# Optimization experiments

Hardware: AMD Instinct MI355X
Metric: run time of the kernel (lower is better)

## Reference

```python
import jax, jax.numpy as jnp
import numpy as np

SPEED_OF_SOUND = 343.0
SAMPLING_FREQUENCY = 96000.0
CROP_LENGTH = 256


def setup_inputs() -> dict:
    key = jax.random.key(0)
    k1, k2, k3, k4 = jax.random.split(key, 4)
    B1, B2, R, T = 4, 1024, 64, 16384
    recordings = jax.random.normal(k1, (B1, R, T), dtype=jnp.float32)
    sample_locations = jax.random.uniform(k2, (B1, B2, 3), dtype=jnp.float32)  # points in unit cube
    emitter_location = jnp.array([0.0, 0.0, 0.5], dtype=jnp.float32)
    receiver_locations = jax.random.uniform(k3, (R, 3), dtype=jnp.float32) * 0.2
    canonical_echo = jax.random.normal(k4, (CROP_LENGTH,), dtype=jnp.float32)
    return {
        "recordings": recordings,
        "sample_locations": sample_locations,
        "emitter_location": emitter_location,
        "receiver_locations": receiver_locations,
        "canonical_echo": canonical_echo,
    }


def _time_of_flight_crop(recordings, sample_locations, emitter_location, receiver_locations):
    # recordings: (B1, R, T); sample_locations: (B1, B2, 3)
    B1, R, T = recordings.shape
    # emitter -> sample distance: (B1, B2)
    d_es = jnp.linalg.norm(sample_locations - emitter_location, axis=-1)
    # sample -> receiver distance: (B1, B2, R)
    d_sr = jnp.linalg.norm(
        sample_locations[:, :, None, :] - receiver_locations[None, None, :, :], axis=-1
    )
    # fractional start sample index of the echo window: (B1, B2, R)
    start = (d_es[:, :, None] + d_sr) / SPEED_OF_SOUND * SAMPLING_FREQUENCY
    # fractional sample indices for the crop window: (B1, B2, R, L)
    idx = start[..., None] + jnp.arange(CROP_LENGTH, dtype=recordings.dtype)
    i0f = jnp.floor(idx)
    frac = idx - i0f
    i0 = jnp.clip(i0f.astype(jnp.int32), 0, T - 1)
    i1 = jnp.clip(i0 + 1, 0, T - 1)
    # gather per (B1, R) row: vmap over B2 so we never broadcast recordings to (B1,B2,R,T)
    gather = jax.vmap(
        lambda i: jnp.take_along_axis(recordings, i, axis=-1), in_axes=1, out_axes=1
    )
    v0 = gather(i0)  # (B1, B2, R, L)
    v1 = gather(i1)
    return v0 * (1.0 - frac) + v1 * frac  # linear interpolation


def reference(recordings, sample_locations, emitter_location, receiver_locations, canonical_echo):
    cropped = _time_of_flight_crop(
        recordings, sample_locations, emitter_location, receiver_locations
    )  # (B1, B2, R, L)
    # dot with canonical echo template over L, clamp at 0, sum over receivers
    products = jnp.einsum("bqrl,l->bqr", cropped, canonical_echo)
    products = jnp.maximum(products, 0.0)
    magnitude = jnp.sum(products, axis=2)  # (B1, B2)
    return magnitude
```

## Files before the change

kernel.cpp:

```cpp
#include <hip/hip_runtime.h>

#define T_LEN 16384
#define R_CNT 64
#define CROP 256
#define B2_CNT 1024
#define QS 128
#define CDW 584
#define CDW_S 656

typedef _Float16 h2 __attribute__((ext_vector_type(2)));

__device__ __forceinline__ h2 as_h2(unsigned u) {
    union { unsigned u; h2 h; } v; v.u = u; return v.h;
}

#if __has_builtin(__builtin_amdgcn_fdot2)
__device__ __forceinline__ float DOT2(unsigned a, unsigned b, float c) {
    return __builtin_amdgcn_fdot2(as_h2(a), as_h2(b), c, false);
}
#else
__device__ __forceinline__ float DOT2(unsigned a, unsigned b, float c) {
    h2 x = as_h2(a), y = as_h2(b);
    return fmaf((float)x[0], (float)y[0], fmaf((float)x[1], (float)y[1], c));
}
#endif

__global__ void zero_out(float* __restrict__ out) {
    out[blockIdx.x * 256 + threadIdx.x] = 0.0f;
}

__global__ __launch_bounds__(256, 6) void tof_kernel(
    const float* __restrict__ recordings,
    const float* __restrict__ sample_locations,
    const float* __restrict__ emitter,
    const float* __restrict__ receivers,
    const float* __restrict__ echo,
    float* __restrict__ out)
{
    const int blk  = blockIdx.x;
    const int b1   = blk >> 9;
    const int r    = (blk >> 3) & 63;
    const int qc   = blk & 7;
    const int tid  = threadIdx.x;
    const int lane = tid & 63;
    const int wave = tid >> 6;
    const int i8   = lane & 7;
    const int g3   = lane >> 3;

    __shared__ unsigned s_copy[8 * CDW_S];
    __shared__ unsigned s_echo_pk[CROP / 2];
    __shared__ float2   s_sf[QS];

    const float* __restrict__ row = recordings + ((size_t)b1 * R_CNT + r) * T_LEN;
    #pragma unroll
    for (int c = 0; c < 8; ++c)
        for (int j = tid; j < CDW; j += 256) {
            const float a = row[c + 2 * j];
            const float b = row[c + 2 * j + 1];
            s_copy[c * CDW_S + j + 4 * (j >> 5)] =
                __builtin_bit_cast(unsigned, __builtin_amdgcn_cvt_pkrtz(a, b));
        }

    if (tid < CROP / 2)
        s_echo_pk[tid] = __builtin_bit_cast(unsigned,
            __builtin_amdgcn_cvt_pkrtz(echo[2 * tid], echo[2 * tid + 1]));

    if (tid < QS) {
        const int q = qc * QS + tid;
        const float sx = sample_locations[(b1 * B2_CNT + q) * 3 + 0];
        const float sy = sample_locations[(b1 * B2_CNT + q) * 3 + 1];
        const float sz = sample_locations[(b1 * B2_CNT + q) * 3 + 2];
        const float ex = emitter[0], ey = emitter[1], ez = emitter[2];
        const float dex = sx - ex, dey = sy - ey, dez = sz - ez;
        const float d_es = sqrtf(fmaf(dex, dex, fmaf(dey, dey, dez * dez)));
        const float rx = receivers[r * 3 + 0];
        const float ry = receivers[r * 3 + 1];
        const float rz = receivers[r * 3 + 2];
        const float dx = sx - rx, dy = sy - ry, dz = sz - rz;
        const float d_sr = sqrtf(fmaf(dx, dx, fmaf(dy, dy, dz * dz)));

        const float SCALE = 96000.0f / 343.0f;
        const float start = (d_es + d_sr) * SCALE;
        const float i0f   = floorf(start);
        int s0 = (int)i0f;
        s0 = s0 < 0 ? 0 : (s0 > 904 ? 904 : s0);
        s_sf[tid] = make_float2(__int_as_float(s0), start - i0f);
    }
    __syncthreads();

    unsigned e[16];
    #pragma unroll
    for (int n = 0; n < 4; ++n)
        *(uint4*)&e[4 * n] = *(const uint4*)&s_echo_pk[i8 * 16 + 4 * n];

    for (int pass = 0; pass < 4; ++pass) {
        const int ql = wave * 32 + pass * 8 + g3;
        const float2 sf  = s_sf[ql];
        const int   s0   = __float_as_int(sf.x);
        const float frac = sf.y;
        const int   c    = s0 & 7;
        const int   D    = 4 * (s0 >> 3) + 16 * i8;

        const unsigned* __restrict__ cb = &s_copy[c * CDW_S];

        unsigned d[17];
        #pragma unroll
        for (int n = 0; n < 4; ++n) {
            const int dj = D + 4 * n;
            *(uint4*)&d[4 * n] = *(const uint4*)&cb[dj + 4 * (dj >> 5)];
        }
        {
            const int dj = D + 16;
            d[16] = cb[dj + 4 * (dj >> 5)];
        }

        float A = 0.0f, B = 0.0f;
        #pragma unroll
        for (int k = 0; k < 16; ++k) {
            A = DOT2(e[k], d[k], A);
            const unsigned sh = (d[k] >> 16) | (d[k + 1] << 16);
            B = DOT2(e[k], sh, B);
        }

        float pr = fmaf(frac, B - A, A);
        pr += __shfl_xor(pr, 1);
        pr += __shfl_xor(pr, 2);
        pr += __shfl_xor(pr, 4);

        if (i8 == 0)
            atomicAdd(&out[b1 * B2_CNT + qc * QS + ql], fmaxf(pr, 0.0f));
    }
}

extern "C" void kernel_launch(void* const* d_in, const int* in_sizes, int n_in,
                              void* d_out, int out_size, void* d_ws, size_t ws_size,
                              hipStream_t stream) {
    const float* recordings       = (const float*)d_in[0];
    const float* sample_locations = (const float*)d_in[1];
    const float* emitter          = (const float*)d_in[2];
    const float* receivers        = (const float*)d_in[3];
    const float* echo             = (const float*)d_in[4];
    float* out                    = (float*)d_out;

    const int B1 = in_sizes[1] / (B2_CNT * 3);

    zero_out<<<dim3(B1 * B2_CNT / 256), dim3(256), 0, stream>>>(out);
    tof_kernel<<<dim3(B1 * R_CNT * 8), dim3(256), 0, stream>>>(
        recordings, sample_locations, emitter, receivers, echo, out);
}
```

Measured before the change: 84.54 us.

## Precompute per-row echo correlation at all lags, then interpolate per sample pair

Interpolation is linear, so the dot product of the echo with an interpolated crop equals the interpolation of two integer-lag correlations. A first kernel computes the correlation of each (b1, r) recording row with the echo at every lag 0..919 and writes it to workspace. A second kernel computes each sample's time of flight and reads two correlation values per receiver. The second kernel sums receivers in shared memory instead of with atomics, which also removes the zero-out launch. The work now scales with the number of lags rather than the number of samples, at the cost of a global round trip through the workspace and a second kernel launch.

```diff
diff --git a/kernel.cpp b/kernel.cpp
--- a/kernel.cpp
+++ b/kernel.cpp
@@ -4,9 +4,9 @@
 #define R_CNT 64
 #define CROP 256
 #define B2_CNT 1024
-#define QS 128
-#define CDW 584
-#define CDW_S 656
+#define CDW 588
+#define CDW_S 664
+#define NLAG 928
 
 typedef _Float16 h2 __attribute__((ext_vector_type(2)));
 
@@ -25,31 +25,23 @@
 }
 #endif
 
-__global__ void zero_out(float* __restrict__ out) {
-    out[blockIdx.x * 256 + threadIdx.x] = 0.0f;
-}
-
-__global__ __launch_bounds__(256, 6) void tof_kernel(
+__global__ __launch_bounds__(256) void corr_kernel(
     const float* __restrict__ recordings,
-    const float* __restrict__ sample_locations,
-    const float* __restrict__ emitter,
-    const float* __restrict__ receivers,
     const float* __restrict__ echo,
-    float* __restrict__ out)
+    float* __restrict__ C)
 {
     const int blk  = blockIdx.x;
-    const int b1   = blk >> 9;
-    const int r    = (blk >> 3) & 63;
-    const int qc   = blk & 7;
+    const int b1   = blk >> 8;
+    const int r    = (blk >> 2) & 63;
+    const int base = (blk & 3) * 256;
     const int tid  = threadIdx.x;
     const int lane = tid & 63;
     const int wave = tid >> 6;
     const int i8   = lane & 7;
     const int g3   = lane >> 3;
 
-    __shared__ unsigned s_copy[8 * CDW_S];
-    __shared__ unsigned s_echo_pk[CROP / 2];
-    __shared__ float2   s_sf[QS];
+    __shared__ __align__(16) unsigned s_copy[8 * CDW_S];
+    __shared__ __align__(16) unsigned s_echo_pk[CROP / 2];
 
     const float* __restrict__ row = recordings + ((size_t)b1 * R_CNT + r) * T_LEN;
     #pragma unroll
@@ -60,32 +52,9 @@
             s_copy[c * CDW_S + j + 4 * (j >> 5)] =
                 __builtin_bit_cast(unsigned, __builtin_amdgcn_cvt_pkrtz(a, b));
         }
-
     if (tid < CROP / 2)
         s_echo_pk[tid] = __builtin_bit_cast(unsigned,
             __builtin_amdgcn_cvt_pkrtz(echo[2 * tid], echo[2 * tid + 1]));
-
-    if (tid < QS) {
-        const int q = qc * QS + tid;
-        const float sx = sample_locations[(b1 * B2_CNT + q) * 3 + 0];
-        const float sy = sample_locations[(b1 * B2_CNT + q) * 3 + 1];
-        const float sz = sample_locations[(b1 * B2_CNT + q) * 3 + 2];
-        const float ex = emitter[0], ey = emitter[1], ez = emitter[2];
-        const float dex = sx - ex, dey = sy - ey, dez = sz - ez;
-        const float d_es = sqrtf(fmaf(dex, dex, fmaf(dey, dey, dez * dez)));
-        const float rx = receivers[r * 3 + 0];
-        const float ry = receivers[r * 3 + 1];
-        const float rz = receivers[r * 3 + 2];
-        const float dx = sx - rx, dy = sy - ry, dz = sz - rz;
-        const float d_sr = sqrtf(fmaf(dx, dx, fmaf(dy, dy, dz * dz)));
-
-        const float SCALE = 96000.0f / 343.0f;
-        const float start = (d_es + d_sr) * SCALE;
-        const float i0f   = floorf(start);
-        int s0 = (int)i0f;
-        s0 = s0 < 0 ? 0 : (s0 > 904 ? 904 : s0);
-        s_sf[tid] = make_float2(__int_as_float(s0), start - i0f);
-    }
     __syncthreads();
 
     unsigned e[16];
@@ -93,42 +62,101 @@
     for (int n = 0; n < 4; ++n)
         *(uint4*)&e[4 * n] = *(const uint4*)&s_echo_pk[i8 * 16 + 4 * n];
 
+    const int s = wave * 8 + g3;
+    float* __restrict__ Crow = C + ((size_t)b1 * R_CNT + r) * NLAG;
+
+    #pragma unroll
     for (int pass = 0; pass < 4; ++pass) {
-        const int ql = wave * 32 + pass * 8 + g3;
-        const float2 sf  = s_sf[ql];
-        const int   s0   = __float_as_int(sf.x);
-        const float frac = sf.y;
-        const int   c    = s0 & 7;
-        const int   D    = 4 * (s0 >> 3) + 16 * i8;
+        const int J = base + pass * 64 + (s & 7) + ((s >> 3) * 16);
+        if (J < 920) {
+            const int c = J & 7;
+            const int b = J >> 3;
+            const unsigned* __restrict__ cb = &s_copy[c * CDW_S];
 
-        const unsigned* __restrict__ cb = &s_copy[c * CDW_S];
+            unsigned d[20];
+            #pragma unroll
+            for (int n = 0; n < 5; ++n) {
+                const int dj = 4 * b + 16 * i8 + 4 * n;
+                *(uint4*)&d[4 * n] = *(const uint4*)&cb[dj + 4 * (dj >> 5)];
+            }
 
-        unsigned d[17];
+            float a0 = 0.0f, a1 = 0.0f;
+            #pragma unroll
+            for (int k = 0; k < 16; ++k) {
+                a0 = DOT2(e[k], d[k],     a0);
+                a1 = DOT2(e[k], d[k + 4], a1);
+            }
+            a0 += __shfl_xor(a0, 1); a1 += __shfl_xor(a1, 1);
+            a0 += __shfl_xor(a0, 2); a1 += __shfl_xor(a1, 2);
+            a0 += __shfl_xor(a0, 4); a1 += __shfl_xor(a1, 4);
+            if (i8 == 0) {
+                Crow[J]     = a0;
+                Crow[J + 8] = a1;
+            }
+        }
+    }
+}
+
+__global__ __launch_bounds__(256) void pair_kernel(
+    const float* __restrict__ sample_locations,
+    const float* __restrict__ emitter,
+    const float* __restrict__ receivers,
+    const float* __restrict__ C,
+    float* __restrict__ out)
+{
+    const int blk = blockIdx.x;
+    const int b1  = blk >> 6;
+    const int qc  = blk & 63;
+    const int tid = threadIdx.x;
+    const int ql  = tid & 15;
+    const int rg  = tid >> 4;
+
+    __shared__ float s_recv[R_CNT * 3];
+    __shared__ float s_part[16][17];
+
+    if (tid < R_CNT * 3) s_recv[tid] = receivers[tid];
+    __syncthreads();
+
+    const int q = qc * 16 + ql;
+    const float sx = sample_locations[(b1 * B2_CNT + q) * 3 + 0];
+    const float sy = sample_locations[(b1 * B2_CNT + q) * 3 + 1];
+    const float sz = sample_locations[(b1 * B2_CNT + q) * 3 + 2];
+    const float ex = emitter[0], ey = emitter[1], ez = emitter[2];
+    const float dex = sx - ex, dey = sy - ey, dez = sz - ez;
+    const float d_es = sqrtf(fmaf(dex, dex, fmaf(dey, dey, dez * dez)));
+
+    const float SCALE = 96000.0f / 343.0f;
+    float acc = 0.0f;
+
+    #pragma unroll
+    for (int rr = 0; rr < 4; ++rr) {
+        const int r = rg * 4 + rr;
+        const float rx = s_recv[r * 3 + 0];
+        const float ry = s_recv[r * 3 + 1];
+        const float rz = s_recv[r * 3 + 2];
+        const float dx = sx - rx, dy = sy - ry, dz = sz - rz;
+        const float d_sr = sqrtf(fmaf(dx, dx, fmaf(dy, dy, dz * dz)));
+
+        const float start = (d_es + d_sr) * SCALE;
+        const float i0f   = floorf(start);
+        const float frac  = start - i0f;
+        int s0 = (int)i0f;
+        s0 = s0 < 0 ? 0 : (s0 > 904 ? 904 : s0);
+
+        const float* cp = C + ((size_t)b1 * R_CNT + r) * NLAG + s0;
+        const float c0 = cp[0];
+        const float c1 = cp[1];
+        acc += fmaxf(fmaf(frac, c1 - c0, c0), 0.0f);
+    }
+
+    s_part[rg][ql] = acc;
+    __syncthreads();
+
+    if (tid < 16) {
+        float sum = 0.0f;
         #pragma unroll
-        for (int n = 0; n < 4; ++n) {
-            const int dj = D + 4 * n;
-            *(uint4*)&d[4 * n] = *(const uint4*)&cb[dj + 4 * (dj >> 5)];
-        }
-        {
-            const int dj = D + 16;
-            d[16] = cb[dj + 4 * (dj >> 5)];
-        }
-
-        float A = 0.0f, B = 0.0f;
-        #pragma unroll
-        for (int k = 0; k < 16; ++k) {
-            A = DOT2(e[k], d[k], A);
-            const unsigned sh = (d[k] >> 16) | (d[k + 1] << 16);
-            B = DOT2(e[k], sh, B);
-        }
-
-        float pr = fmaf(frac, B - A, A);
-        pr += __shfl_xor(pr, 1);
-        pr += __shfl_xor(pr, 2);
-        pr += __shfl_xor(pr, 4);
-
-        if (i8 == 0)
-            atomicAdd(&out[b1 * B2_CNT + qc * QS + ql], fmaxf(pr, 0.0f));
+        for (int g = 0; g < 16; ++g) sum += s_part[g][tid];
+        out[b1 * B2_CNT + qc * 16 + tid] = sum;
     }
 }
 
@@ -141,10 +169,11 @@
     const float* receivers        = (const float*)d_in[3];
     const float* echo             = (const float*)d_in[4];
     float* out                    = (float*)d_out;
+    float* C                      = (float*)d_ws;
 
     const int B1 = in_sizes[1] / (B2_CNT * 3);
 
-    zero_out<<<dim3(B1 * B2_CNT / 256), dim3(256), 0, stream>>>(out);
-    tof_kernel<<<dim3(B1 * R_CNT * 8), dim3(256), 0, stream>>>(
-        recordings, sample_locations, emitter, receivers, echo, out);
+    corr_kernel<<<dim3(B1 * R_CNT * 4), dim3(256), 0, stream>>>(recordings, echo, C);
+    pair_kernel<<<dim3(B1 * 64), dim3(256), 0, stream>>>(sample_locations, emitter,
+                                                         receivers, C, out);
 }
```

After: 77.70 us. 8.1% less time.

## Precompute per-row cross-correlation lags and interpolate per sample

Applied to the files above, without the earlier changes.

Instead of computing a 256-tap dot product for each (sample, receiver) pair, each block now computes the correlation of the echo template with the recording row at every integer lag (920 lags) once into shared memory. Each sample point then linearly interpolates between two adjacent lag values. This works because the dot product is linear, so interpolation commutes with it. The block count drops from 8 to 2 per (b1, r) row. Staging now uses vectorized float4 loads that fill all eight shifted copies. The cost is computing all lags even if unused (920 vs 1024 samples per row), and lower grid parallelism (512 blocks).

```diff
diff --git a/kernel.cpp b/kernel.cpp
--- a/kernel.cpp
+++ b/kernel.cpp
@@ -4,14 +4,18 @@
 #define R_CNT 64
 #define CROP 256
 #define B2_CNT 1024
-#define QS 128
-#define CDW 584
-#define CDW_S 656
+#define CDW 596
+#define CDW_S 676
+#define NLAG 928
 
 typedef _Float16 h2 __attribute__((ext_vector_type(2)));
 
 __device__ __forceinline__ h2 as_h2(unsigned u) {
     union { unsigned u; h2 h; } v; v.u = u; return v.h;
+}
+
+__device__ __forceinline__ unsigned pk(float a, float b) {
+    return __builtin_bit_cast(unsigned, __builtin_amdgcn_cvt_pkrtz(a, b));
 }
 
 #if __has_builtin(__builtin_amdgcn_fdot2)
@@ -29,7 +33,7 @@
     out[blockIdx.x * 256 + threadIdx.x] = 0.0f;
 }
 
-__global__ __launch_bounds__(256, 6) void tof_kernel(
+__global__ __launch_bounds__(256) void tof_fused(
     const float* __restrict__ recordings,
     const float* __restrict__ sample_locations,
     const float* __restrict__ emitter,
@@ -38,54 +42,43 @@
     float* __restrict__ out)
 {
     const int blk  = blockIdx.x;
-    const int b1   = blk >> 9;
-    const int r    = (blk >> 3) & 63;
-    const int qc   = blk & 7;
+    const int b1   = blk >> 7;
+    const int r    = (blk >> 1) & 63;
+    const int h    = blk & 1;
     const int tid  = threadIdx.x;
     const int lane = tid & 63;
     const int wave = tid >> 6;
     const int i8   = lane & 7;
     const int g3   = lane >> 3;
 
-    __shared__ unsigned s_copy[8 * CDW_S];
-    __shared__ unsigned s_echo_pk[CROP / 2];
-    __shared__ float2   s_sf[QS];
+    __shared__ __align__(16) unsigned s_copy[8 * CDW_S];
+    __shared__ __align__(16) unsigned s_echo_pk[CROP / 2];
+    __shared__ __align__(16) float    s_lag[NLAG];
 
     const float* __restrict__ row = recordings + ((size_t)b1 * R_CNT + r) * T_LEN;
-    #pragma unroll
-    for (int c = 0; c < 8; ++c)
-        for (int j = tid; j < CDW; j += 256) {
-            const float a = row[c + 2 * j];
-            const float b = row[c + 2 * j + 1];
-            s_copy[c * CDW_S + j + 4 * (j >> 5)] =
-                __builtin_bit_cast(unsigned, __builtin_amdgcn_cvt_pkrtz(a, b));
+
+    if (tid < 150) {
+        const float4 wa = *reinterpret_cast<const float4*>(&row[8 * tid]);
+        const float4 wb = *reinterpret_cast<const float4*>(&row[8 * tid + 4]);
+        const float  we = row[8 * tid + 8];
+        const unsigned u[4] = { pk(wa.x, wa.y), pk(wa.z, wa.w), pk(wb.x, wb.y), pk(wb.z, wb.w) };
+        const unsigned v[4] = { pk(wa.y, wa.z), pk(wa.w, wb.x), pk(wb.y, wb.z), pk(wb.w, we) };
+        const int k0 = 4 * tid;
+        #pragma unroll
+        for (int d = 0; d < 4; ++d) {
+            #pragma unroll
+            for (int i = 0; i < 4; ++i) {
+                const int j = k0 + i - d;
+                if (j >= 0 && j < CDW) {
+                    const int sj = j + 4 * (j >> 5);
+                    s_copy[(2 * d)     * CDW_S + sj] = u[i];
+                    s_copy[(2 * d + 1) * CDW_S + sj] = v[i];
+                }
+            }
         }
-
+    }
     if (tid < CROP / 2)
-        s_echo_pk[tid] = __builtin_bit_cast(unsigned,
-            __builtin_amdgcn_cvt_pkrtz(echo[2 * tid], echo[2 * tid + 1]));
-
-    if (tid < QS) {
-        const int q = qc * QS + tid;
-        const float sx = sample_locations[(b1 * B2_CNT + q) * 3 + 0];
-        const float sy = sample_locations[(b1 * B2_CNT + q) * 3 + 1];
-        const float sz = sample_locations[(b1 * B2_CNT + q) * 3 + 2];
-        const float ex = emitter[0], ey = emitter[1], ez = emitter[2];
-        const float dex = sx - ex, dey = sy - ey, dez = sz - ez;
-        const float d_es = sqrtf(fmaf(dex, dex, fmaf(dey, dey, dez * dez)));
-        const float rx = receivers[r * 3 + 0];
-        const float ry = receivers[r * 3 + 1];
-        const float rz = receivers[r * 3 + 2];
-        const float dx = sx - rx, dy = sy - ry, dz = sz - rz;
-        const float d_sr = sqrtf(fmaf(dx, dx, fmaf(dy, dy, dz * dz)));
-
-        const float SCALE = 96000.0f / 343.0f;
-        const float start = (d_es + d_sr) * SCALE;
-        const float i0f   = floorf(start);
-        int s0 = (int)i0f;
-        s0 = s0 < 0 ? 0 : (s0 > 904 ? 904 : s0);
-        s_sf[tid] = make_float2(__int_as_float(s0), start - i0f);
-    }
+        s_echo_pk[tid] = pk(echo[2 * tid], echo[2 * tid + 1]);
     __syncthreads();
 
     unsigned e[16];
@@ -93,42 +86,70 @@
     for (int n = 0; n < 4; ++n)
         *(uint4*)&e[4 * n] = *(const uint4*)&s_echo_pk[i8 * 16 + 4 * n];
 
-    for (int pass = 0; pass < 4; ++pass) {
-        const int ql = wave * 32 + pass * 8 + g3;
-        const float2 sf  = s_sf[ql];
-        const int   s0   = __float_as_int(sf.x);
-        const float frac = sf.y;
-        const int   c    = s0 & 7;
-        const int   D    = 4 * (s0 >> 3) + 16 * i8;
+    #pragma unroll 2
+    for (int pass = 0; pass < 8; ++pass) {
+        const int b  = pass * 16 + wave * 4;
+        const int Jl = 8 * b + g3;
+        if (Jl < 920) {
+            const unsigned* __restrict__ cb = &s_copy[g3 * CDW_S];
+            unsigned d[28];
+            #pragma unroll
+            for (int n = 0; n < 7; ++n) {
+                const int dj = 4 * b + 16 * i8 + 4 * n;
+                *(uint4*)&d[4 * n] = *(const uint4*)&cb[dj + 4 * (dj >> 5)];
+            }
+            float a0 = 0.0f, a1 = 0.0f, a2 = 0.0f, a3 = 0.0f;
+            #pragma unroll
+            for (int k = 0; k < 16; ++k) {
+                a0 = DOT2(e[k], d[k],      a0);
+                a1 = DOT2(e[k], d[k + 4],  a1);
+                a2 = DOT2(e[k], d[k + 8],  a2);
+                a3 = DOT2(e[k], d[k + 12], a3);
+            }
+            #pragma unroll
+            for (int off = 1; off <= 4; off <<= 1) {
+                a0 += __shfl_xor(a0, off);
+                a1 += __shfl_xor(a1, off);
+                a2 += __shfl_xor(a2, off);
+                a3 += __shfl_xor(a3, off);
+            }
+            if (i8 == 0) {
+                s_lag[Jl] = a0;
+                if (Jl + 8  < 920) s_lag[Jl + 8]  = a1;
+                if (Jl + 16 < 920) s_lag[Jl + 16] = a2;
+                if (Jl + 24 < 920) s_lag[Jl + 24] = a3;
+            }
+        }
+    }
+    __syncthreads();
 
-        const unsigned* __restrict__ cb = &s_copy[c * CDW_S];
+    const float ex = emitter[0], ey = emitter[1], ez = emitter[2];
+    const float rx = receivers[r * 3 + 0];
+    const float ry = receivers[r * 3 + 1];
+    const float rz = receivers[r * 3 + 2];
+    const float SCALE = 96000.0f / 343.0f;
 
-        unsigned d[17];
-        #pragma unroll
-        for (int n = 0; n < 4; ++n) {
-            const int dj = D + 4 * n;
-            *(uint4*)&d[4 * n] = *(const uint4*)&cb[dj + 4 * (dj >> 5)];
-        }
-        {
-            const int dj = D + 16;
-            d[16] = cb[dj + 4 * (dj >> 5)];
-        }
+    #pragma unroll
+    for (int ii = 0; ii < 2; ++ii) {
+        const int q = h * 512 + ii * 256 + tid;
+        const float sx = sample_locations[(b1 * B2_CNT + q) * 3 + 0];
+        const float sy = sample_locations[(b1 * B2_CNT + q) * 3 + 1];
+        const float sz = sample_locations[(b1 * B2_CNT + q) * 3 + 2];
 
-        float A = 0.0f, B = 0.0f;
-        #pragma unroll
-        for (int k = 0; k < 16; ++k) {
-            A = DOT2(e[k], d[k], A);
-            const unsigned sh = (d[k] >> 16) | (d[k + 1] << 16);
-            B = DOT2(e[k], sh, B);
-        }
+        const float dex = sx - ex, dey = sy - ey, dez = sz - ez;
+        const float d_es = sqrtf(fmaf(dex, dex, fmaf(dey, dey, dez * dez)));
+        const float dx = sx - rx, dy = sy - ry, dz = sz - rz;
+        const float d_sr = sqrtf(fmaf(dx, dx, fmaf(dy, dy, dz * dz)));
 
-        float pr = fmaf(frac, B - A, A);
-        pr += __shfl_xor(pr, 1);
-        pr += __shfl_xor(pr, 2);
-        pr += __shfl_xor(pr, 4);
+        const float start = (d_es + d_sr) * SCALE;
+        const float i0f   = floorf(start);
+        const float frac  = start - i0f;
+        int s0 = (int)i0f;
+        s0 = s0 < 0 ? 0 : (s0 > 904 ? 904 : s0);
 
-        if (i8 == 0)
-            atomicAdd(&out[b1 * B2_CNT + qc * QS + ql], fmaxf(pr, 0.0f));
+        const float c0 = s_lag[s0];
+        const float c1 = s_lag[s0 + 1];
+        atomicAdd(&out[b1 * B2_CNT + q], fmaxf(fmaf(frac, c1 - c0, c0), 0.0f));
     }
 }
 
@@ -145,6 +166,6 @@
     const int B1 = in_sizes[1] / (B2_CNT * 3);
 
     zero_out<<<dim3(B1 * B2_CNT / 256), dim3(256), 0, stream>>>(out);
-    tof_kernel<<<dim3(B1 * R_CNT * 8), dim3(256), 0, stream>>>(
+    tof_fused<<<dim3(B1 * R_CNT * 2), dim3(256), 0, stream>>>(
         recordings, sample_locations, emitter, receivers, echo, out);
 }
```

New measurement: 78.04 us. 1.08x faster.
